# Kernel optimization log

Measured on AMD Instinct MI355X. Metric: run time of the kernel, lower is better.

## Reference

```python
import jax, jax.numpy as jnp
import numpy as np

D = 1e-16  # matches module-level `d` in the torch source


def setup_inputs() -> dict:
    key = jax.random.key(0)
    k1, k2, k3, k4, k5 = jax.random.split(key, 5)
    B, C, H, W = 8, 64, 192, 320
    x = jax.random.normal(k1, (B, C, H, W), dtype=jnp.float32)
    # physically plausible camera params (scaled uniforms)
    h_cam = 1.2 + 0.6 * jax.random.uniform(k2, (B,), dtype=jnp.float32)
    p_cam = 0.15 + 0.15 * jax.random.uniform(k3, (B,), dtype=jnp.float32)
    fu = 250.0 + 100.0 * jax.random.uniform(k4, (B,), dtype=jnp.float32)
    fv = 250.0 + 100.0 * jax.random.uniform(k5, (B,), dtype=jnp.float32)
    return {"x": x, "h_cam": h_cam, "p_cam": p_cam, "fu": fu, "fv": fv, "plane_height": 0}


def _bev_forward(x, h_cam, p_cam, fu, fv, plane_h):
    B, C, H, W = x.shape
    cu, cv = W / 2.0, H / 2.0
    h_ref = h_cam - plane_h
    sp, cp = jnp.sin(p_cam), jnp.cos(p_cam)
    z = jnp.zeros_like(h_cam)

    # world -> image homography, (B, 3, 3)
    row0 = jnp.stack([cu * cp, -fu, cu * h_ref * sp], -1)
    row1 = jnp.stack([cv * cp - fv * sp, z, h_ref * (fv * cp + cv * sp)], -1)
    row2 = jnp.stack([cp, z, h_ref * sp], -1)
    mats = jnp.stack([row0, row1, row2], 1)

    # BEV scales and centers
    scales = h_cam / (sp * (cv * cp + fv * sp) + D)          # (B,)
    centers = jnp.stack([h_cam * cp / (sp + D), z, jnp.ones_like(h_cam)], -1)  # (B, 3)

    # BEV grid (flattened, row-major over (v, u)), N = H*W
    vv, uu = jnp.meshgrid(jnp.arange(H, dtype=x.dtype), jnp.arange(W, dtype=x.dtype), indexing="ij")
    u = uu.reshape(-1)
    v = vv.reshape(-1)

    # bev_coord -> world_coord
    s = scales[:, None]
    wx = centers[:, 0:1] + s * (cv - v[None, :])   # (B, N)
    wy = centers[:, 1:2] + s * (cu - u[None, :])
    world = jnp.stack([wx, wy, jnp.ones_like(wx)], 1)  # (B, 3, N)

    # world_coord -> image_coord (homogeneous divide)
    uvw = jnp.einsum("bij,bjn->bin", mats, world)
    su = uvw[:, 0] / uvw[:, 2]   # sampled u, (B, N)
    sv = uvw[:, 1] / uvw[:, 2]   # sampled v, (B, N)

    # bilinear interpolation with clamped corner indices (as in the torch code,
    # weights are computed from the CLAMPED integer coordinates)
    u0i = jnp.clip(jnp.floor(su).astype(jnp.int32), 0, W - 1)
    u1i = jnp.clip(jnp.floor(su).astype(jnp.int32) + 1, 0, W - 1)
    v0i = jnp.clip(jnp.floor(sv).astype(jnp.int32), 0, H - 1)
    v1i = jnp.clip(jnp.floor(sv).astype(jnp.int32) + 1, 0, H - 1)
    u0f, u1f = u0i.astype(x.dtype), u1i.astype(x.dtype)
    v0f, v1f = v0i.astype(x.dtype), v1i.astype(x.dtype)

    xf = x.reshape(B, C, H * W)

    def gather(vi, ui):
        idx = vi * W + ui                       # (B, N)
        return jnp.take_along_axis(xf, idx[:, None, :], axis=2)  # (B, C, N)

    wa = ((v1f - sv) * (u1f - su))[:, None, :]
    wb = ((sv - v0f) * (u1f - su))[:, None, :]
    wc = ((v1f - sv) * (su - u0f))[:, None, :]
    wd = ((sv - v0f) * (su - u0f))[:, None, :]

    vals = (wa * gather(v0i, u0i) + wb * gather(v1i, u0i)
            + wc * gather(v0i, u1i) + wd * gather(v1i, u1i))
    out = vals.reshape(B, C, H, W)
    return out, scales, centers


def reference(x, h_cam, p_cam, fu, fv, plane_height):
    return _bev_forward(x, h_cam, p_cam, fu, fv, float(plane_height))
```

## Files before the change

### kernel.cpp

```cpp
#include <hip/hip_runtime.h>

#define B_ 8
#define C_ 64
#define H_ 192
#define W_ 320
#define HW_ (H_*W_)
#define OUT_ELEMS ((size_t)B_*C_*H_*W_)

#define CSPLIT 8
#define CPB    (C_/CSPLIT)
#define CGRP   4
#define PIXT   4
#define XTILES (HW_/(256*PIXT))
#define NWG    (XTILES * B_ * CSPLIT)
#define NXCD   8

typedef float f32x4 __attribute__((ext_vector_type(4)));

struct __attribute__((packed, aligned(4))) fpair { float lo, hi; };

__global__ void bev_setup_kernel(const float* __restrict__ h_cam,
                                 const float* __restrict__ p_cam,
                                 const float* __restrict__ fu,
                                 const float* __restrict__ fv,
                                 const int*   __restrict__ plane_h,
                                 double* __restrict__ params,
                                 float*  __restrict__ scales_out,
                                 float*  __restrict__ centers_out) {
    int b = threadIdx.x;
    if (b >= B_) return;
    const double D  = 1e-16;
    const double cu = W_ / 2.0;
    const double cv = H_ / 2.0;
    double h   = (double)h_cam[b];
    double p   = (double)p_cam[b];
    double dfu = (double)fu[b];
    double dfv = (double)fv[b];
    double ph  = (double)plane_h[0];
    double h_ref = h - ph;
    double sp = sin(p), cp = cos(p);

    double m00 = cu * cp;
    double m01 = -dfu;
    double m02 = cu * h_ref * sp;
    double m10 = cv * cp - dfv * sp;
    double m12 = h_ref * (dfv * cp + cv * sp);
    double m20 = cp;
    double m22 = h_ref * sp;
    double s   = h / (sp * (cv * cp + dfv * sp) + D);
    double cx  = h * cp / (sp + D);

    double* pp = params + (size_t)b * 10;
    pp[0] = m00; pp[1] = m01; pp[2] = m02;
    pp[3] = m10; pp[4] = m12;
    pp[5] = m20; pp[6] = m22;
    pp[7] = s;   pp[8] = cx;

    scales_out[b] = (float)s;
    centers_out[b*3 + 0] = (float)cx;
    centers_out[b*3 + 1] = 0.0f;
    centers_out[b*3 + 2] = 1.0f;
}

__global__ __launch_bounds__(256, 4)
void bev_main_kernel(const float* __restrict__ x,
                     const double* __restrict__ params,
                     float* __restrict__ out) {
    const int wg    = blockIdx.x;
    const int newid = (wg % NXCD) * (NWG / NXCD) + (wg / NXCD);
    const int bc    = newid / XTILES;
    const int xt    = newid - bc * XTILES;
    const int b     = bc >> 3;
    const int c0    = (bc & 7) * CPB;
    const int pix0  = (xt * 256 + threadIdx.x) * PIXT;
    const int v     = pix0 / W_;
    const int u     = pix0 - v * W_;

    const double* pp = params + (size_t)b * 10;
    const double m00 = pp[0], m01 = pp[1], m02 = pp[2];
    const double m10 = pp[3], m12 = pp[4];
    const double m20 = pp[5], m22 = pp[6];
    const double s   = pp[7], cx  = pp[8];

    const double wx     = cx + s * ((double)(H_/2) - (double)v);
    const double t2     = m20 * wx + m22;
    const double inv_t2 = 1.0 / t2;
    const double sv     = (m10 * wx + m12) * inv_t2;
    const double su_c   = (m00 * wx + m02) * inv_t2;
    const double su_k   = m01 * s * inv_t2;

    const bool rowin = (sv >= 0.0) && (sv < (double)(H_-1));
    int v0i = 0;
    float dv0 = 0.f, dv1 = 0.f;
    if (rowin) {
        v0i = (int)sv;
        dv0 = (float)(sv - (double)v0i);
        dv1 = (float)((double)(v0i + 1) - sv);
    }

    float wa[PIXT], wb[PIXT], wc[PIXT], wd[PIXT];
    int   base[PIXT];
    #pragma unroll
    for (int k = 0; k < PIXT; ++k) {
        const double su = su_c + su_k * ((double)(W_/2) - (double)(u + k));
        const bool inr = rowin && (su >= 0.0) && (su < (double)(W_-1));
        int u0i = 0;
        float du0 = 0.f, du1 = 0.f;
        if (inr) {
            u0i = (int)su;
            du0 = (float)(su - (double)u0i);
            du1 = (float)((double)(u0i + 1) - su);
        }
        wa[k] = dv1 * du1;
        wb[k] = dv0 * du1;
        wc[k] = dv1 * du0;
        wd[k] = dv0 * du0;
        base[k] = v0i * W_ + u0i;
    }

    const float* __restrict__ xb = x   + ((size_t)(b * C_ + c0)) * HW_;
    float* __restrict__       ob = out + ((size_t)(b * C_ + c0)) * HW_ + (size_t)pix0;

    #pragma unroll
    for (int g = 0; g < CPB / CGRP; ++g) {
        fpair tp[CGRP][PIXT], bp[CGRP][PIXT];
        #pragma unroll
        for (int c = 0; c < CGRP; ++c) {
            const float* __restrict__ xc = xb + (size_t)(g * CGRP + c) * HW_;
            #pragma unroll
            for (int k = 0; k < PIXT; ++k) {
                tp[c][k] = *(const fpair*)(xc + base[k]);
                bp[c][k] = *(const fpair*)(xc + base[k] + W_);
            }
        }
        #pragma unroll
        for (int c = 0; c < CGRP; ++c) {
            f32x4 r;
            r.x = wa[0]*tp[c][0].lo + wc[0]*tp[c][0].hi + wb[0]*bp[c][0].lo + wd[0]*bp[c][0].hi;
            r.y = wa[1]*tp[c][1].lo + wc[1]*tp[c][1].hi + wb[1]*bp[c][1].lo + wd[1]*bp[c][1].hi;
            r.z = wa[2]*tp[c][2].lo + wc[2]*tp[c][2].hi + wb[2]*bp[c][2].lo + wd[2]*bp[c][2].hi;
            r.w = wa[3]*tp[c][3].lo + wc[3]*tp[c][3].hi + wb[3]*bp[c][3].lo + wd[3]*bp[c][3].hi;
            __builtin_nontemporal_store(r, (f32x4*)(ob + (size_t)(g * CGRP + c) * HW_));
        }
    }
}

extern "C" void kernel_launch(void* const* d_in, const int* in_sizes, int n_in,
                              void* d_out, int out_size, void* d_ws, size_t ws_size,
                              hipStream_t stream) {
    const float* x     = (const float*)d_in[0];
    const float* h_cam = (const float*)d_in[1];
    const float* p_cam = (const float*)d_in[2];
    const float* fu    = (const float*)d_in[3];
    const float* fv    = (const float*)d_in[4];
    const int*   ph    = (const int*)  d_in[5];

    float* out = (float*)d_out;
    float* scales_out  = out + OUT_ELEMS;
    float* centers_out = out + OUT_ELEMS + B_;
    double* params = (double*)d_ws;

    bev_setup_kernel<<<1, 64, 0, stream>>>(h_cam, p_cam, fu, fv, ph,
                                           params, scales_out, centers_out);

    bev_main_kernel<<<NWG, 256, 0, stream>>>(x, params, out);
}
```

Before: 44.54 us.

## Remap threads so adjacent lanes own adjacent pixels with strided scalar stores

Each workgroup now covers four full image rows with 320 threads. Each thread handles four pixels spaced 80 columns apart instead of four contiguous pixels, so neighbouring lanes read neighbouring gather addresses and write coalesced scalar stores. The channel loop walks one channel at a time with unroll 2, in place of groups of four channels with 16-byte vector stores. This aims to improve gather coalescing, at the cost of giving up vector stores and lowering memory-level parallelism per thread.

```diff
diff --git a/kernel.cpp b/kernel.cpp
--- a/kernel.cpp
+++ b/kernel.cpp
@@ -9,9 +9,9 @@
 
 #define CSPLIT 8
 #define CPB    (C_/CSPLIT)
-#define CGRP   4
-#define PIXT   4
-#define XTILES (HW_/(256*PIXT))
+#define NTHR   320
+#define ROWSPB 4
+#define XTILES (H_/ROWSPB)
 #define NWG    (XTILES * B_ * CSPLIT)
 #define NXCD   8
 
@@ -62,7 +62,7 @@
     centers_out[b*3 + 2] = 1.0f;
 }
 
-__global__ __launch_bounds__(256, 4)
+__global__ __launch_bounds__(NTHR)
 void bev_main_kernel(const float* __restrict__ x,
                      const double* __restrict__ params,
                      float* __restrict__ out) {
@@ -72,9 +72,11 @@
     const int xt    = newid - bc * XTILES;
     const int b     = bc >> 3;
     const int c0    = (bc & 7) * CPB;
-    const int pix0  = (xt * 256 + threadIdx.x) * PIXT;
-    const int v     = pix0 / W_;
-    const int u     = pix0 - v * W_;
+
+    const int t  = threadIdx.x;
+    const int rg = t / 80;
+    const int u0 = t - rg * 80;
+    const int v  = xt * ROWSPB + rg;
 
     const double* pp = params + (size_t)b * 10;
     const double m00 = pp[0], m01 = pp[1], m02 = pp[2];
@@ -98,11 +100,11 @@
         dv1 = (float)((double)(v0i + 1) - sv);
     }
 
-    float wa[PIXT], wb[PIXT], wc[PIXT], wd[PIXT];
-    int   base[PIXT];
+    float wa[4], wb[4], wc[4], wd[4];
+    int   base[4];
     #pragma unroll
-    for (int k = 0; k < PIXT; ++k) {
-        const double su = su_c + su_k * ((double)(W_/2) - (double)(u + k));
+    for (int j = 0; j < 4; ++j) {
+        const double su = su_c + su_k * ((double)(W_/2) - (double)(u0 + 80*j));
         const bool inr = rowin && (su >= 0.0) && (su < (double)(W_-1));
         int u0i = 0;
         float du0 = 0.f, du1 = 0.f;
@@ -111,36 +113,32 @@
             du0 = (float)(su - (double)u0i);
             du1 = (float)((double)(u0i + 1) - su);
         }
-        wa[k] = dv1 * du1;
-        wb[k] = dv0 * du1;
-        wc[k] = dv1 * du0;
-        wd[k] = dv0 * du0;
-        base[k] = v0i * W_ + u0i;
+        wa[j] = dv1 * du1;
+        wb[j] = dv0 * du1;
+        wc[j] = dv1 * du0;
+        wd[j] = dv0 * du0;
+        base[j] = v0i * W_ + u0i;
     }
 
     const float* __restrict__ xb = x   + ((size_t)(b * C_ + c0)) * HW_;
-    float* __restrict__       ob = out + ((size_t)(b * C_ + c0)) * HW_ + (size_t)pix0;
+    float* __restrict__       ob = out + ((size_t)(b * C_ + c0)) * HW_
+                                       + (size_t)v * W_ + (size_t)u0;
 
-    #pragma unroll
-    for (int g = 0; g < CPB / CGRP; ++g) {
-        fpair tp[CGRP][PIXT], bp[CGRP][PIXT];
+    #pragma unroll 2
+    for (int c = 0; c < CPB; ++c) {
+        const float* __restrict__ xc = xb + (size_t)c * HW_;
+        float* __restrict__       oc = ob + (size_t)c * HW_;
+        fpair tp[4], bp[4];
         #pragma unroll
-        for (int c = 0; c < CGRP; ++c) {
-            const float* __restrict__ xc = xb + (size_t)(g * CGRP + c) * HW_;
-            #pragma unroll
-            for (int k = 0; k < PIXT; ++k) {
-                tp[c][k] = *(const fpair*)(xc + base[k]);
-                bp[c][k] = *(const fpair*)(xc + base[k] + W_);
-            }
+        for (int j = 0; j < 4; ++j) {
+            tp[j] = *(const fpair*)(xc + base[j]);
+            bp[j] = *(const fpair*)(xc + base[j] + W_);
         }
         #pragma unroll
-        for (int c = 0; c < CGRP; ++c) {
-            f32x4 r;
-            r.x = wa[0]*tp[c][0].lo + wc[0]*tp[c][0].hi + wb[0]*bp[c][0].lo + wd[0]*bp[c][0].hi;
-            r.y = wa[1]*tp[c][1].lo + wc[1]*tp[c][1].hi + wb[1]*bp[c][1].lo + wd[1]*bp[c][1].hi;
-            r.z = wa[2]*tp[c][2].lo + wc[2]*tp[c][2].hi + wb[2]*bp[c][2].lo + wd[2]*bp[c][2].hi;
-            r.w = wa[3]*tp[c][3].lo + wc[3]*tp[c][3].hi + wb[3]*bp[c][3].lo + wd[3]*bp[c][3].hi;
-            __builtin_nontemporal_store(r, (f32x4*)(ob + (size_t)(g * CGRP + c) * HW_));
+        for (int j = 0; j < 4; ++j) {
+            const float r = wa[j]*tp[j].lo + wc[j]*tp[j].hi
+                          + wb[j]*bp[j].lo + wd[j]*bp[j].hi;
+            __builtin_nontemporal_store(r, oc + 80*j);
         }
     }
 }
@@ -163,5 +161,5 @@
     bev_setup_kernel<<<1, 64, 0, stream>>>(h_cam, p_cam, fu, fv, ph,
                                            params, scales_out, centers_out);
 
-    bev_main_kernel<<<NWG, 256, 0, stream>>>(x, params, out);
+    bev_main_kernel<<<NWG, NTHR, 0, stream>>>(x, params, out);
 }
```

Measured after the change: 46.43 us. 1.04x slower.
